# Optimization experiments

Hardware: AMD Instinct MI355X
Metric: run time of the kernel (lower is better)

Reference implementation:

```python
import jax, jax.numpy as jnp
import numpy as np

B, V = 128, 128000
N_GREEDY = 8  # rows with temperature == 0 to exercise the argmax fallback


def setup_inputs() -> dict:
    key = jax.random.key(0)
    k1, k2, k3, k4 = jax.random.split(key, 4)
    logits = jax.random.normal(k1, (B, V), dtype=jnp.float32)
    temperatures = jax.random.uniform(k2, (B, 1), dtype=jnp.float32, minval=0.1, maxval=1.5)
    temperatures = temperatures.at[:N_GREEDY].set(0.0)  # greedy rows
    top_ps = 0.5 + 0.5 * jax.random.uniform(k3, (B, 1), dtype=jnp.float32)  # in [0.5, 1.0]
    top_ks = jax.random.randint(k4, (B, 1), 1, 64).astype(jnp.float32)  # stored as float, like torch code
    return {"logits": logits, "temperatures": temperatures, "top_ps": top_ps, "top_ks": top_ks}


def reference(logits, temperatures, top_ps, top_ks):
    # Temperature scale (temp==0 rows use safe temperature 1.0, overridden by greedy below)
    safe_t = jnp.where(temperatures == 0.0, 1.0, temperatures)  # [B,1]
    scaled = logits / safe_t  # [B,V] -- this is the `probs` returned by the torch module

    probs = jax.nn.softmax(scaled, axis=-1)  # [B,V]

    # Descending sort over vocab
    order = jnp.argsort(-probs, axis=-1)                      # [B,V] int
    sorted_probs = jnp.take_along_axis(probs, order, axis=-1)  # [B,V]
    cum = jnp.cumsum(sorted_probs, axis=-1)                    # [B,V]

    ranks = jnp.arange(V, dtype=jnp.float32)[None, :]          # [1,V]
    keep_k = ranks < top_ks                                    # top-k mask  [B,V]
    keep_p = (cum - sorted_probs) < top_ps                     # top-p mask (cumprob before token < p)
    keep = (keep_k & keep_p) | (ranks == 0.0)                  # always keep the top-1 token

    # Joint filter + Gumbel-max sampling (equivalent to renormalize-then-categorical)
    logp = jnp.where(keep, jnp.log(sorted_probs), -jnp.inf)    # [B,V]
    g = jax.random.gumbel(jax.random.key(42), (B, V), dtype=jnp.float32)
    sampled_sorted = jnp.argmax(logp + g, axis=-1)             # [B] index in sorted space
    sampled = jnp.take_along_axis(order, sampled_sorted[:, None], axis=-1)[:, 0]  # back to vocab ids

    # Greedy fallback for temperature == 0 rows (argmax of ORIGINAL logits)
    greedy = jnp.argmax(logits, axis=-1)
    ids = jnp.where(temperatures[:, 0] == 0.0, greedy, sampled).astype(jnp.int32)

    return ids, scaled
```

## Files before the change

kernel.cpp:

```cpp
#include <hip/hip_runtime.h>
#include <stdint.h>

#define NB 128
#define NV 128000
#define TOPC 63

#define JPB 25
#define CH 5120
#define CH4 1280
#define K1T 256
#define QPT 5
#define HB 8192
#define HBW (HB / 2)
#define WINSD 2.2f
#define CSLOT 104
#define SCCAP (JPB * CSLOT)
#define NHB 2048
#define SNCAP 256
#define NBLK1 (NB * JPB)

#define WS_CS_OFF   0
#define WS_CS_BYTES ((size_t)NBLK1 * CSLOT * 4)
#define WS_M_OFF    (WS_CS_BYTES)
#define WS_S_OFF    (WS_M_OFF + NBLK1 * 4)
#define WS_CNT_OFF  (WS_S_OFF + NBLK1 * 4)
#define WS_CTR_OFF  (WS_CNT_OFF + NBLK1 * 4)
#define WS_CI_OFF   (WS_CTR_OFF + NB * 4)
#define WS_NEED     (WS_CI_OFF + (size_t)NBLK1 * CSLOT * 2)

#define NT 1024
#define NV4 (NV / 4)
#define NBINS 16384
#define CCAP 2048

typedef float f4 __attribute__((ext_vector_type(4)));

__device__ __forceinline__ uint32_t rotl32(uint32_t v, uint32_t d) {
  return (v << d) | (v >> (32u - d));
}

__device__ __forceinline__ void threefry2x32(uint32_t k0, uint32_t k1,
                                             uint32_t x0, uint32_t x1,
                                             uint32_t& o0, uint32_t& o1) {
  uint32_t ks2 = k0 ^ k1 ^ 0x1BD11BDAu;
  x0 += k0; x1 += k1;
#define TF_ROUND(r) { x0 += x1; x1 = rotl32(x1, (r)); x1 ^= x0; }
  TF_ROUND(13) TF_ROUND(15) TF_ROUND(26) TF_ROUND(6)
  x0 += k1;  x1 += ks2 + 1u;
  TF_ROUND(17) TF_ROUND(29) TF_ROUND(16) TF_ROUND(24)
  x0 += ks2; x1 += k0 + 2u;
  TF_ROUND(13) TF_ROUND(15) TF_ROUND(26) TF_ROUND(6)
  x0 += k0;  x1 += k1 + 3u;
  TF_ROUND(17) TF_ROUND(29) TF_ROUND(16) TF_ROUND(24)
  x0 += k1;  x1 += ks2 + 4u;
  TF_ROUND(13) TF_ROUND(15) TF_ROUND(26) TF_ROUND(6)
  x0 += ks2; x1 += k0 + 5u;
#undef TF_ROUND
  o0 = x0; o1 = x1;
}

__device__ __forceinline__ uint32_t jax_random_bits_u32(uint64_t n) {
  uint32_t o0, o1;
  threefry2x32(0u, 42u, (uint32_t)(n >> 32), (uint32_t)n, o0, o1);
  return o0 ^ o1;
}

__device__ __forceinline__ float gumbel_from_bits(uint32_t bits) {
  const float tiny = 1.17549435e-38f;
  float f = __uint_as_float(0x3f800000u | (bits >> 9)) - 1.0f;
  float u = f * 1.0f + tiny;
  u = fmaxf(tiny, u);
  return -logf(-logf(u));
}

__device__ __forceinline__ uint32_t sortkey(float x) {
  uint32_t b = __float_as_uint(x);
  uint32_t mask = (uint32_t)((int32_t)b >> 31) | 0x80000000u;
  return b ^ mask;
}

__device__ __forceinline__ float div_exact(float a, float st, float ry) {
  float q0 = a * ry;
  float r  = __builtin_fmaf(-st, q0, a);
  return __builtin_fmaf(r, ry, q0);
}

__global__ __launch_bounds__(K1T) void k1_scan(
    const float* __restrict__ logits, const float* __restrict__ temps,
    float* __restrict__ out, uint32_t* __restrict__ cand_s,
    uint16_t* __restrict__ cand_i, float* __restrict__ m_arr,
    float* __restrict__ S_arr, uint32_t* __restrict__ cnt_arr) {

  __shared__ uint32_t histw[HBW];
  __shared__ uint32_t ssum[K1T];
  __shared__ float swm[4], sws[4];
  __shared__ uint32_t wtot[4];
  __shared__ int s_tstar;
  __shared__ uint32_t s_cutbin, s_cutkey, s_lcnt;

  const int bid = blockIdx.x;
  const int r = bid / JPB, j = bid - r * JPB;
  const int t = threadIdx.x;
  const int lane = t & 63, wv = t >> 6;
  const float temp = temps[r];
  const float st = (temp == 0.0f) ? 1.0f : temp;
  const float ry = 1.0f / st;

  const f4* __restrict__ lrow4 = (const f4*)(logits + (size_t)r * NV + (size_t)j * CH);
  f4* __restrict__ srow4 = (f4*)(out + NB + (size_t)r * NV + (size_t)j * CH);

  histw[t] = 0u;
  if (t == 0) { s_lcnt = 0u; s_tstar = K1T - 1; s_cutbin = 255u; }

  f4 sreg[QPT];
  float mx0 = -INFINITY, mx1 = -INFINITY, mx2 = -INFINITY, mx3 = -INFINITY;
  float sm0 = 0.0f, sm1 = 0.0f, sm2 = 0.0f, sm3 = 0.0f;
  #pragma unroll
  for (int q = 0; q < QPT; ++q) {
    int i = q * K1T + t;
    f4 x = lrow4[i];
    f4 s;
    s.x = div_exact(x.x, st, ry);
    s.y = div_exact(x.y, st, ry);
    s.z = div_exact(x.z, st, ry);
    s.w = div_exact(x.w, st, ry);
    srow4[i] = s;
    sreg[q] = s;
    mx0 = fmaxf(mx0, s.x); mx1 = fmaxf(mx1, s.y);
    mx2 = fmaxf(mx2, s.z); mx3 = fmaxf(mx3, s.w);
    sm0 += __expf(s.x); sm1 += __expf(s.y);
    sm2 += __expf(s.z); sm3 += __expf(s.w);
  }
  float mx = fmaxf(fmaxf(mx0, mx1), fmaxf(mx2, mx3));
  float sum = (sm0 + sm1) + (sm2 + sm3);
  #pragma unroll
  for (int off = 32; off > 0; off >>= 1) {
    mx = fmaxf(mx, __shfl_xor(mx, off));
    sum += __shfl_xor(sum, off);
  }
  if (lane == 0) { swm[wv] = mx; sws[wv] = sum; }
  __syncthreads();
  const float mxb = fmaxf(fmaxf(swm[0], swm[1]), fmaxf(swm[2], swm[3]));
  if (t == 0) {
    m_arr[bid] = mxb;
    S_arr[bid] = sws[0] + sws[1] + sws[2] + sws[3];
  }
  const float F = (256.0f / WINSD) * st;

  #pragma unroll
  for (int q = 0; q < QPT; ++q) {
    float sv[4] = {sreg[q].x, sreg[q].y, sreg[q].z, sreg[q].w};
    #pragma unroll
    for (int c = 0; c < 4; ++c) {
      float d = (mxb - sv[c]) * F;
      if (d < 256.0f) atomicAdd(&histw[(uint32_t)d], 1u);
    }
  }
  __syncthreads();

  {
    uint32_t c = histw[t];
    uint32_t ps = c;
    #pragma unroll
    for (int off = 1; off < 64; off <<= 1) {
      uint32_t v = __shfl_up(ps, off);
      if (lane >= off) ps += v;
    }
    if (lane == 63) wtot[wv] = ps;
    __syncthreads();
    uint32_t add = 0;
    #pragma unroll
    for (int w2 = 0; w2 < 4; ++w2)
      if (w2 < wv) add += wtot[w2];
    ps += add;
    if (ps >= 63u && (ps - c) < 63u) s_cutbin = (uint32_t)t;
  }
  __syncthreads();
  const uint32_t cutbin = s_cutbin;

  uint32_t* __restrict__ mys = cand_s + (size_t)bid * CSLOT;
  uint16_t* __restrict__ myi = cand_i + (size_t)bid * CSLOT;
  #pragma unroll
  for (int q = 0; q < QPT; ++q) {
    float sv[4] = {sreg[q].x, sreg[q].y, sreg[q].z, sreg[q].w};
    #pragma unroll
    for (int c = 0; c < 4; ++c) {
      float d = (mxb - sv[c]) * F;
      if (d < 256.0f && (uint32_t)d <= cutbin) {
        uint32_t pos = atomicAdd(&s_lcnt, 1u);
        if (pos < CSLOT) {
          mys[pos] = __float_as_uint(sv[c]);
          myi[pos] = (uint16_t)((q * K1T + t) * 4 + c);
        }
      }
    }
  }
  __syncthreads();
  const uint32_t lc = s_lcnt;
  if (lc >= 63u && lc <= (uint32_t)CSLOT) {
    if (t == 0) cnt_arr[bid] = lc;
    return;
  }

  if (t == 0) s_lcnt = 0u;
  for (int i = t; i < HBW; i += K1T) histw[i] = 0u;
  __syncthreads();
  #pragma unroll
  for (int q = 0; q < QPT; ++q) {
    float sv[4] = {sreg[q].x, sreg[q].y, sreg[q].z, sreg[q].w};
    #pragma unroll
    for (int c = 0; c < 4; ++c) {
      uint32_t b = sortkey(sv[c]) >> 19;
      atomicAdd(&histw[b >> 1], (b & 1) ? 65536u : 1u);
    }
  }
  __syncthreads();
  uint32_t sloc = 0;
  #pragma unroll
  for (int u = 0; u < 16; ++u) {
    uint32_t w = histw[t * 16 + u];
    sloc += (w & 0xFFFFu) + (w >> 16);
  }
  ssum[t] = sloc;
  __syncthreads();
  for (int off = 1; off < K1T; off <<= 1) {
    uint32_t v = ssum[t] + ((t + off < K1T) ? ssum[t + off] : 0u);
    __syncthreads();
    ssum[t] = v;
    __syncthreads();
  }
  if (ssum[t] >= 63u && (t == K1T - 1 || ssum[t + 1] < 63u)) s_tstar = t;
  __syncthreads();
  if (t == 0) {
    int ts = s_tstar;
    uint32_t running = (ts == K1T - 1) ? 0u : ssum[ts + 1];
    int cb = ts * 32;
    for (int q = 31; q >= 0; --q) {
      uint32_t w = histw[ts * 16 + (q >> 1)];
      uint32_t c = (q & 1) ? (w >> 16) : (w & 0xFFFFu);
      running += c;
      if (running >= 63u) { cb = ts * 32 + q; break; }
    }
    s_cutkey = (uint32_t)cb << 19;
  }
  __syncthreads();
  const uint32_t cutkey = s_cutkey;
  #pragma unroll
  for (int q = 0; q < QPT; ++q) {
    float sv[4] = {sreg[q].x, sreg[q].y, sreg[q].z, sreg[q].w};
    #pragma unroll
    for (int c = 0; c < 4; ++c) {
      if (sortkey(sv[c]) >= cutkey) {
        uint32_t pos = atomicAdd(&s_lcnt, 1u);
        if (pos < CSLOT) {
          mys[pos] = __float_as_uint(sv[c]);
          myi[pos] = (uint16_t)((q * K1T + t) * 4 + c);
        }
      }
    }
  }
  __syncthreads();
  if (t == 0) cnt_arr[bid] = (s_lcnt < CSLOT) ? s_lcnt : (uint32_t)CSLOT;
}

__global__ __launch_bounds__(K1T) void k2_final(
    const float* __restrict__ temps, const float* __restrict__ topps,
    const float* __restrict__ topks, const uint32_t* __restrict__ cand_s,
    const uint16_t* __restrict__ cand_i, const float* __restrict__ m_arr,
    const float* __restrict__ S_arr, const uint32_t* __restrict__ cnt_arr,
    float* __restrict__ out) {

  __shared__ unsigned long long sc[SCCAP];
  __shared__ uint32_t nhist[NHB];
  __shared__ unsigned long long sn[SNCAP];
  __shared__ float sm8[32], ss8[32];
  __shared__ uint32_t scnt8[JPB];
  __shared__ uint32_t swsum[4];
  __shared__ uint32_t s_cutp, s_scnt;
  __shared__ float s_m, s_Z;
  __shared__ float sp[TOPC], scum[TOPC], slv[TOPC];
  __shared__ int sidx_[TOPC];

  const int r = blockIdx.x;
  const int t = threadIdx.x;
  const int lane = t & 63, wv = t >> 6;
  const float temp = temps[r];

  if (t < 32) {
    sm8[t] = (t < JPB) ? m_arr[r * JPB + t] : -INFINITY;
    ss8[t] = (t < JPB) ? S_arr[r * JPB + t] : 0.0f;
  }
  if (t < JPB) scnt8[t] = cnt_arr[r * JPB + t];
  for (int i = t; i < NHB; i += K1T) nhist[i] = 0u;
  __syncthreads();
  if (t == 0) {
    float m = -INFINITY;
    for (int q = 0; q < JPB; ++q) m = fmaxf(m, sm8[q]);
    float Sr = 0.0f;
    for (int q = 0; q < JPB; ++q) Sr += ss8[q];
    s_m = m;
    s_Z = Sr * expf(-m);
    s_scnt = 0u;
  }
  __syncthreads();
  const float m = s_m, Z = s_Z;

  for (int e = t; e < SCCAP; e += K1T) {
    int q = e / CSLOT;
    int slot = e - q * CSLOT;
    if (slot < (int)scnt8[q]) {
      int gs = (r * JPB + q) * CSLOT + slot;
      float s = __uint_as_float(cand_s[gs]);
      uint32_t idx = (uint32_t)q * CH + (uint32_t)cand_i[gs];
      float p = expf(s - m) / Z;
      sc[e] = ((unsigned long long)__float_as_uint(p) << 32)
            | (unsigned long long)(0xFFFFFFFFu - idx);
      atomicAdd(&nhist[__float_as_uint(p) >> 21], 1u);
    }
  }
  __syncthreads();

  uint32_t nloc = 0;
  #pragma unroll
  for (int u = 0; u < 8; ++u) nloc += nhist[t * 8 + u];
  uint32_t ns = nloc;
  #pragma unroll
  for (int off = 1; off < 64; off <<= 1) {
    uint32_t v = __shfl_down(ns, off);
    if (lane + off < 64) ns += v;
  }
  if (lane == 0) swsum[wv] = ns;
  __syncthreads();
  #pragma unroll
  for (int w2 = 0; w2 < 4; ++w2)
    if (w2 > wv) ns += swsum[w2];
  if (ns >= 63u && (ns - nloc) < 63u) {
    uint32_t running = ns - nloc;
    int cutbin = t * 8;
    for (int u = 7; u >= 0; --u) {
      running += nhist[t * 8 + u];
      if (running >= 63u) { cutbin = t * 8 + u; break; }
    }
    s_cutp = (uint32_t)cutbin << 21;
  }
  __syncthreads();
  const uint32_t cutp = s_cutp;

  for (int e = t; e < SCCAP; e += K1T) {
    int q = e / CSLOT;
    int slot = e - q * CSLOT;
    if (slot < (int)scnt8[q]) {
      unsigned long long v = sc[e];
      if ((uint32_t)(v >> 32) >= cutp) {
        uint32_t pos = atomicAdd(&s_scnt, 1u);
        if (pos < SNCAP) sn[pos] = v;
      }
    }
  }
  __syncthreads();
  const uint32_t scnt = s_scnt;
  if (t < SNCAP && t >= (int)scnt) sn[t] = 0ull;
  __syncthreads();

  for (int k = 2; k <= SNCAP; k <<= 1) {
    for (int jj = k >> 1; jj > 0; jj >>= 1) {
      int e = t;
      int ixj = e ^ jj;
      if (ixj > e) {
        unsigned long long a = sn[e], c = sn[ixj];
        bool desc = ((e & k) == 0);
        if (desc ? (a < c) : (a > c)) { sn[e] = c; sn[ixj] = a; }
      }
      __syncthreads();
    }
  }

  if (t < TOPC) {
    unsigned long long kv = sn[t];
    sp[t] = __uint_as_float((uint32_t)(kv >> 32));
    sidx_[t] = (int)(0xFFFFFFFFu - (uint32_t)(kv & 0xFFFFFFFFull));
  }
  __syncthreads();
  if (t == 0) {
    float L0[63], L1[31], L2[15], L3[7], L4[3];
    for (int i = 0; i < 63; ++i) L0[i] = sp[i];
    for (int i = 0; i < 31; ++i) L1[i] = L0[2*i] + L0[2*i+1];
    for (int i = 0; i < 15; ++i) L2[i] = L1[2*i] + L1[2*i+1];
    for (int i = 0; i < 7;  ++i) L3[i] = L2[2*i] + L2[2*i+1];
    for (int i = 0; i < 3;  ++i) L4[i] = L3[2*i] + L3[2*i+1];
    float S5 = L4[0] + L4[1];
    float S4[3]; S4[0] = L4[0]; S4[1] = S5; S4[2] = S5 + L4[2];
    float S3[7]; S3[0] = L3[0];
    for (int k = 0; k < 3; ++k) { S3[2*k+1] = S4[k]; if (2*k+2 < 7)  S3[2*k+2] = S4[k] + L3[2*k+2]; }
    float S2[15]; S2[0] = L2[0];
    for (int k = 0; k < 7; ++k) { S2[2*k+1] = S3[k]; if (2*k+2 < 15) S2[2*k+2] = S3[k] + L2[2*k+2]; }
    float S1[31]; S1[0] = L1[0];
    for (int k = 0; k < 15; ++k){ S1[2*k+1] = S2[k]; if (2*k+2 < 31) S1[2*k+2] = S2[k] + L1[2*k+2]; }
    scum[0] = L0[0];
    for (int k = 0; k < 31; ++k){ scum[2*k+1] = S1[k]; if (2*k+2 < 63) scum[2*k+2] = S1[k] + L0[2*k+2]; }
  }
  __syncthreads();
  if (t < TOPC) {
    const float topp = topps[r];
    const float topk = topks[r];
    bool keep = (((float)t < topk) && ((scum[t] - sp[t]) < topp)) || (t == 0);
    uint32_t bits = jax_random_bits_u32((uint64_t)r * NV + (uint64_t)t);
    float g = gumbel_from_bits(bits);
    slv[t] = keep ? (logf(sp[t]) + g) : -INFINITY;
  }
  __syncthreads();
  if (t == 0) {
    float best = slv[0]; int br = 0;
    for (int q = 1; q < TOPC; ++q)
      if (slv[q] > best) { best = slv[q]; br = q; }
    int id = (temp == 0.0f) ? sidx_[0] : sidx_[br];
    out[r] = (float)id;
  }
}


__global__ __launch_bounds__(NT) void sampler_kernel(
    const float* __restrict__ logits, const float* __restrict__ temps,
    const float* __restrict__ topps, const float* __restrict__ topks,
    float* __restrict__ out) {

  __shared__ union {
    uint32_t hist[NBINS];
    unsigned long long cand[CCAP];
  } sh;
  __shared__ uint32_t ssum[NT];
  __shared__ float redf[NT];
  __shared__ uint32_t s_cutkey, s_cnt;
  __shared__ int s_tstar;
  __shared__ float sp[TOPC], scum[TOPC], slv[TOPC];
  __shared__ int sidx_[TOPC];

  const int b = blockIdx.x;
  const int t = threadIdx.x;
  const float temp = temps[b];
  const float st = (temp == 0.0f) ? 1.0f : temp;
  const float topp = topps[b];
  const float topk = topks[b];

  const float4* __restrict__ lrow = (const float4*)(logits + (size_t)b * NV);
  float4* __restrict__ srow = (float4*)(out + NB + (size_t)b * NV);

  for (int i = t; i < NBINS; i += NT) sh.hist[i] = 0u;
  if (t == 0) s_tstar = NT - 1;

  float lmax = -INFINITY;
  for (int i = t; i < NV4; i += NT) {
    float4 x = lrow[i];
    float4 s;
    s.x = x.x / st; s.y = x.y / st; s.z = x.z / st; s.w = x.w / st;
    srow[i] = s;
    lmax = fmaxf(lmax, fmaxf(fmaxf(s.x, s.y), fmaxf(s.z, s.w)));
  }
  redf[t] = lmax;
  __syncthreads();
  for (int off = NT / 2; off > 0; off >>= 1) {
    if (t < off) redf[t] = fmaxf(redf[t], redf[t + off]);
    __syncthreads();
  }
  const float m = redf[0];
  __syncthreads();

  float lsum = 0.0f;
  for (int i = t; i < NV4; i += NT) {
    float4 x = lrow[i];
    float s0 = x.x / st, s1 = x.y / st, s2 = x.z / st, s3 = x.w / st;
    lsum += expf(s0 - m); lsum += expf(s1 - m);
    lsum += expf(s2 - m); lsum += expf(s3 - m);
    atomicAdd(&sh.hist[sortkey(s0) >> 18], 1u);
    atomicAdd(&sh.hist[sortkey(s1) >> 18], 1u);
    atomicAdd(&sh.hist[sortkey(s2) >> 18], 1u);
    atomicAdd(&sh.hist[sortkey(s3) >> 18], 1u);
  }
  redf[t] = lsum;
  __syncthreads();
  for (int off = NT / 2; off > 0; off >>= 1) {
    if (t < off) redf[t] += redf[t + off];
    __syncthreads();
  }
  const float Z = redf[0];
  __syncthreads();

  uint32_t sloc = 0;
  #pragma unroll
  for (int j = 0; j < 16; ++j) sloc += sh.hist[t * 16 + j];
  ssum[t] = sloc;
  __syncthreads();
  for (int off = 1; off < NT; off <<= 1) {
    uint32_t v = ssum[t] + ((t + off < NT) ? ssum[t + off] : 0u);
    __syncthreads();
    ssum[t] = v;
    __syncthreads();
  }
  if (ssum[t] >= 63u && (t == NT - 1 || ssum[t + 1] < 63u)) s_tstar = t;
  __syncthreads();
  if (t == 0) {
    int ts = s_tstar;
    uint32_t running = (ts == NT - 1) ? 0u : ssum[ts + 1];
    int cutbin = ts * 16;
    for (int j = 15; j >= 0; --j) {
      running += sh.hist[ts * 16 + j];
      if (running >= 63u) { cutbin = ts * 16 + j; break; }
    }
    s_cutkey = (uint32_t)cutbin << 18;
    s_cnt = 0u;
  }
  __syncthreads();
  const uint32_t cutkey = s_cutkey;

  for (int i = t; i < NV4; i += NT) {
    float4 x = lrow[i];
    float sv[4];
    sv[0] = x.x / st; sv[1] = x.y / st; sv[2] = x.z / st; sv[3] = x.w / st;
    #pragma unroll
    for (int j = 0; j < 4; ++j) {
      uint32_t key = sortkey(sv[j]);
      if (key >= cutkey) {
        float p = expf(sv[j] - m) / Z;
        uint32_t pos = atomicAdd(&s_cnt, 1u);
        if (pos < CCAP) {
          uint32_t idx = (uint32_t)(i * 4 + j);
          sh.cand[pos] = ((unsigned long long)__float_as_uint(p) << 32)
                       | (unsigned long long)(0xFFFFFFFFu - idx);
        }
      }
    }
  }
  __syncthreads();
  const uint32_t cnt = s_cnt;
  for (int e = t; e < CCAP; e += NT)
    if ((uint32_t)e >= cnt) sh.cand[e] = 0ull;
  __syncthreads();

  for (uint32_t k = 2; k <= CCAP; k <<= 1) {
    for (uint32_t j = k >> 1; j > 0; j >>= 1) {
      for (int e = t; e < CCAP; e += NT) {
        uint32_t ixj = (uint32_t)e ^ j;
        if (ixj > (uint32_t)e) {
          unsigned long long a = sh.cand[e], c = sh.cand[ixj];
          bool desc = (((uint32_t)e & k) == 0u);
          if (desc ? (a < c) : (a > c)) { sh.cand[e] = c; sh.cand[ixj] = a; }
        }
      }
      __syncthreads();
    }
  }

  if (t < TOPC) {
    unsigned long long kv = sh.cand[t];
    sp[t] = __uint_as_float((uint32_t)(kv >> 32));
    sidx_[t] = (int)(0xFFFFFFFFu - (uint32_t)(kv & 0xFFFFFFFFull));
  }
  __syncthreads();
  if (t == 0) {
    float L0[63], L1[31], L2[15], L3[7], L4[3];
    for (int i = 0; i < 63; ++i) L0[i] = sp[i];
    for (int i = 0; i < 31; ++i) L1[i] = L0[2*i] + L0[2*i+1];
    for (int i = 0; i < 15; ++i) L2[i] = L1[2*i] + L1[2*i+1];
    for (int i = 0; i < 7;  ++i) L3[i] = L2[2*i] + L2[2*i+1];
    for (int i = 0; i < 3;  ++i) L4[i] = L3[2*i] + L3[2*i+1];
    float S5 = L4[0] + L4[1];
    float S4[3]; S4[0] = L4[0]; S4[1] = S5; S4[2] = S5 + L4[2];
    float S3[7]; S3[0] = L3[0];
    for (int k = 0; k < 3; ++k) { S3[2*k+1] = S4[k]; if (2*k+2 < 7)  S3[2*k+2] = S4[k] + L3[2*k+2]; }
    float S2[15]; S2[0] = L2[0];
    for (int k = 0; k < 7; ++k) { S2[2*k+1] = S3[k]; if (2*k+2 < 15) S2[2*k+2] = S3[k] + L2[2*k+2]; }
    float S1[31]; S1[0] = L1[0];
    for (int k = 0; k < 15; ++k){ S1[2*k+1] = S2[k]; if (2*k+2 < 31) S1[2*k+2] = S2[k] + L1[2*k+2]; }
    scum[0] = L0[0];
    for (int k = 0; k < 31; ++k){ scum[2*k+1] = S1[k]; if (2*k+2 < 63) scum[2*k+2] = S1[k] + L0[2*k+2]; }
  }
  __syncthreads();
  if (t < TOPC) {
    bool keep = (((float)t < topk) && ((scum[t] - sp[t]) < topp)) || (t == 0);
    uint32_t bits = jax_random_bits_u32((uint64_t)b * NV + (uint64_t)t);
    float g = gumbel_from_bits(bits);
    slv[t] = keep ? (logf(sp[t]) + g) : -INFINITY;
  }
  __syncthreads();
  if (t == 0) {
    float best = slv[0]; int br = 0;
    for (int q = 1; q < TOPC; ++q)
      if (slv[q] > best) { best = slv[q]; br = q; }
    int id = (temp == 0.0f) ? sidx_[0] : sidx_[br];
    out[b] = (float)id;
  }
}

extern "C" void kernel_launch(void* const* d_in, const int* in_sizes, int n_in,
                              void* d_out, int out_size, void* d_ws, size_t ws_size,
                              hipStream_t stream) {
  const float* logits = (const float*)d_in[0];
  const float* temps  = (const float*)d_in[1];
  const float* topps  = (const float*)d_in[2];
  const float* topks  = (const float*)d_in[3];
  float* out = (float*)d_out;

  if (ws_size >= WS_NEED) {
    uint32_t* cand_s  = (uint32_t*)((char*)d_ws + WS_CS_OFF);
    uint16_t* cand_i  = (uint16_t*)((char*)d_ws + WS_CI_OFF);
    float*    m_arr   = (float*)((char*)d_ws + WS_M_OFF);
    float*    S_arr   = (float*)((char*)d_ws + WS_S_OFF);
    uint32_t* cnt_arr = (uint32_t*)((char*)d_ws + WS_CNT_OFF);
    hipLaunchKernelGGL(k1_scan, dim3(NBLK1), dim3(K1T), 0, stream,
                       logits, temps, out, cand_s, cand_i, m_arr, S_arr, cnt_arr);
    hipLaunchKernelGGL(k2_final, dim3(NB), dim3(K1T), 0, stream,
                       temps, topps, topks, cand_s, cand_i,
                       m_arr, S_arr, cnt_arr, out);
  } else {
    hipLaunchKernelGGL(sampler_kernel, dim3(NB), dim3(NT), 0, stream,
                       logits, temps, topps, topks, out);
  }
}
```

Before: 49.14 us.

## Split scale-and-store into separate kernel and re-read scaled logits for selection

The fused scan kernel is split into two kernels. The first only reads logits, divides by temperature and writes the scaled output. The second re-reads the scaled values from global memory (likely from L2/MALL) to compute the max, the exp-sum and the candidate selection. The apparent aim is to let the streaming kernel run at full bandwidth without the register and LDS pressure of the selection code. The cost is an extra kernel launch and about 65 MB of extra reads.

```diff
diff --git a/kernel.cpp b/kernel.cpp
--- a/kernel.cpp
+++ b/kernel.cpp
@@ -85,36 +85,17 @@
   return __builtin_fmaf(r, ry, q0);
 }
 
-__global__ __launch_bounds__(K1T) void k1_scan(
+__global__ __launch_bounds__(K1T) void k0_stream(
     const float* __restrict__ logits, const float* __restrict__ temps,
-    float* __restrict__ out, uint32_t* __restrict__ cand_s,
-    uint16_t* __restrict__ cand_i, float* __restrict__ m_arr,
-    float* __restrict__ S_arr, uint32_t* __restrict__ cnt_arr) {
-
-  __shared__ uint32_t histw[HBW];
-  __shared__ uint32_t ssum[K1T];
-  __shared__ float swm[4], sws[4];
-  __shared__ uint32_t wtot[4];
-  __shared__ int s_tstar;
-  __shared__ uint32_t s_cutbin, s_cutkey, s_lcnt;
-
+    float* __restrict__ out) {
   const int bid = blockIdx.x;
   const int r = bid / JPB, j = bid - r * JPB;
   const int t = threadIdx.x;
-  const int lane = t & 63, wv = t >> 6;
   const float temp = temps[r];
   const float st = (temp == 0.0f) ? 1.0f : temp;
   const float ry = 1.0f / st;
-
   const f4* __restrict__ lrow4 = (const f4*)(logits + (size_t)r * NV + (size_t)j * CH);
   f4* __restrict__ srow4 = (f4*)(out + NB + (size_t)r * NV + (size_t)j * CH);
-
-  histw[t] = 0u;
-  if (t == 0) { s_lcnt = 0u; s_tstar = K1T - 1; s_cutbin = 255u; }
-
-  f4 sreg[QPT];
-  float mx0 = -INFINITY, mx1 = -INFINITY, mx2 = -INFINITY, mx3 = -INFINITY;
-  float sm0 = 0.0f, sm1 = 0.0f, sm2 = 0.0f, sm3 = 0.0f;
   #pragma unroll
   for (int q = 0; q < QPT; ++q) {
     int i = q * K1T + t;
@@ -125,7 +106,46 @@
     s.z = div_exact(x.z, st, ry);
     s.w = div_exact(x.w, st, ry);
     srow4[i] = s;
-    sreg[q] = s;
+  }
+}
+
+__global__ __launch_bounds__(K1T) void k1_select(
+    const float* __restrict__ out_scaled, const float* __restrict__ temps,
+    uint32_t* __restrict__ cand_s, uint16_t* __restrict__ cand_i,
+    float* __restrict__ m_arr, float* __restrict__ S_arr,
+    uint32_t* __restrict__ cnt_arr) {
+
+  __shared__ uint32_t histw[HBW];
+  __shared__ uint32_t ssum[K1T];
+  __shared__ float swm[4], sws[4];
+  __shared__ uint32_t wtot[4];
+  __shared__ int s_tstar;
+  __shared__ uint32_t s_cutbin, s_cutkey, s_lcnt;
+
+  const int bid = blockIdx.x;
+  const int r = bid / JPB, j = bid - r * JPB;
+  const int t = threadIdx.x;
+  const int lane = t & 63, wv = t >> 6;
+  const float temp = temps[r];
+  const float st = (temp == 0.0f) ? 1.0f : temp;
+  const float ry = 1.0f / st;
+
+  const f4* __restrict__ srow4 =
+      (const f4*)(out_scaled + NB + (size_t)r * NV + (size_t)j * CH);
+
+  histw[t] = 0u;
+  if (t == 0) { s_lcnt = 0u; s_tstar = K1T - 1; s_cutbin = 255u; }
+
+  f4 sreg[QPT];
+  #pragma unroll
+  for (int q = 0; q < QPT; ++q)
+    sreg[q] = srow4[q * K1T + t];
+
+  float mx0 = -INFINITY, mx1 = -INFINITY, mx2 = -INFINITY, mx3 = -INFINITY;
+  float sm0 = 0.0f, sm1 = 0.0f, sm2 = 0.0f, sm3 = 0.0f;
+  #pragma unroll
+  for (int q = 0; q < QPT; ++q) {
+    f4 s = sreg[q];
     mx0 = fmaxf(mx0, s.x); mx1 = fmaxf(mx1, s.y);
     mx2 = fmaxf(mx2, s.z); mx3 = fmaxf(mx3, s.w);
     sm0 += __expf(s.x); sm1 += __expf(s.y);
@@ -606,8 +626,10 @@
     float*    m_arr   = (float*)((char*)d_ws + WS_M_OFF);
     float*    S_arr   = (float*)((char*)d_ws + WS_S_OFF);
     uint32_t* cnt_arr = (uint32_t*)((char*)d_ws + WS_CNT_OFF);
-    hipLaunchKernelGGL(k1_scan, dim3(NBLK1), dim3(K1T), 0, stream,
-                       logits, temps, out, cand_s, cand_i, m_arr, S_arr, cnt_arr);
+    hipLaunchKernelGGL(k0_stream, dim3(NBLK1), dim3(K1T), 0, stream,
+                       logits, temps, out);
+    hipLaunchKernelGGL(k1_select, dim3(NBLK1), dim3(K1T), 0, stream,
+                       out, temps, cand_s, cand_i, m_arr, S_arr, cnt_arr);
     hipLaunchKernelGGL(k2_final, dim3(NB), dim3(K1T), 0, stream,
                        temps, topps, topks, cand_s, cand_i,
                        m_arr, S_arr, cnt_arr, out);
```

Measured after the change: 61.79 us. 1.26x slower.
